# Optimization experiments

Measured on AMD Instinct MI355X. Metric: run time of the kernel, lower is better.

The kernel has to match this reference:

```python
import jax, jax.numpy as jnp
import numpy as np

VOCAB = 8192  # upper bound on integer values appearing in features


def setup_inputs() -> dict:
    key = jax.random.key(0)
    # [B, L] integer codes; each row is treated as a SET of values (duplicates ignored)
    features = jax.random.randint(key, (4096, 256), 0, VOCAB, dtype=jnp.int32)
    return {"features": features}


def reference(features) -> jnp.ndarray:
    # np.intersect1d / np.union1d compute set intersection/union of unique values.
    # Equivalent vectorized form: binary presence matrix P[i, v] = 1 iff value v in row i.
    B, L = features.shape
    rows = jnp.arange(B)[:, None]                                  # [B, 1]
    presence = jnp.zeros((B, VOCAB), jnp.float32).at[rows, features].set(1.0)  # [B, V]
    inter = presence @ presence.T                                  # [B, B] |A_i & A_j|
    sizes = presence.sum(axis=1)                                   # [B]    |A_i|
    union = sizes[:, None] + sizes[None, :] - inter                # [B, B] |A_i | A_j|
    # original returns -intersection/union (note the negation), 0 when union == 0
    sim = jnp.where(union != 0, -inter / jnp.where(union != 0, union, 1.0), 0.0)
    return sim
```

## Files before the change

### kernel.cpp

```cpp
#include <hip/hip_runtime.h>
#include <stdint.h>

#define B_ROWS 4096
#define L_FEAT 256
#define VOCAB  8192
#define FRAG   1024
#define KCHUNKS (VOCAB / 64)
#define GBYTES  (KCHUNKS * FRAG)
#define NSTEP  128

typedef __attribute__((ext_vector_type(4)))  int   intx4;
typedef __attribute__((ext_vector_type(8)))  int   intx8;
typedef __attribute__((ext_vector_type(4)))  float floatx4;
typedef __attribute__((ext_vector_type(16))) float floatx16;

__device__ __forceinline__ intx8 widen(intx4 v) {
  return __builtin_shufflevector(v, v, 0, 1, 2, 3, -1, -1, -1, -1);
}

__global__ __launch_bounds__(256) void presence_kernel(
    const int* __restrict__ f,
    uint32_t* __restrict__ P,
    float* __restrict__ sizes) {
  __shared__ uint32_t rw[4][VOCAB / 8];
  const int rbase = blockIdx.x * 4;
  const int tid = threadIdx.x;

  uint4* rp4 = (uint4*)&rw[0][0];
  const uint4 z = make_uint4(0u, 0u, 0u, 0u);
  #pragma unroll
  for (int j = 0; j < 4; ++j) rp4[tid + j * 256] = z;
  __syncthreads();

  #pragma unroll
  for (int r = 0; r < 4; ++r) {
    const int v = f[(rbase + r) * L_FEAT + tid];
    atomicOr(&rw[r][v >> 3], 0x2u << ((v & 7) * 4));
  }
  __syncthreads();

  const int g = blockIdx.x >> 3;
  const int slotBase = (blockIdx.x & 7) * 4;
  char* Pg = (char*)P + (size_t)g * GBYTES;
  #pragma unroll
  for (int j = 0; j < 4; ++j) {
    const int c  = tid + j * 256;
    const int kc = c >> 3, h = (c >> 2) & 1, ro = c & 3;
    const uint4 val = *(const uint4*)&rw[ro][kc * 8 + h * 4];
    *(uint4*)(Pg + kc * FRAG + (slotBase + ro + 32 * h) * 16) = val;
  }

  const int w = tid >> 6, lane = tid & 63;
  const uint4* sp4 = (const uint4*)&rw[w][0];
  int cnt = 0;
  #pragma unroll
  for (int q = 0; q < 4; ++q) {
    const uint4 x = sp4[lane + q * 64];
    cnt += __popc(x.x & 0x22222222u) + __popc(x.y & 0x22222222u) +
           __popc(x.z & 0x22222222u) + __popc(x.w & 0x22222222u);
  }
  #pragma unroll
  for (int off = 32; off > 0; off >>= 1) cnt += __shfl_down(cnt, off);
  if (lane == 0) sizes[rbase + w] = (float)cnt;
}

__global__ __launch_bounds__(256, 2) void gemm_kernel(
    const unsigned char* __restrict__ P,
    const float* __restrict__ sizes,
    float* __restrict__ out) {
  int bid = blockIdx.x;
  bid = (bid & 7) * 66 + (bid >> 3);
  int b = bid, sy = 0, rem = 122;
  while (b >= rem) { b -= rem; ++sy; rem -= 16; }
  int by, bx;
  if (b < 10) {
    int ly = 0, r2 = 4;
    while (b >= r2) { b -= r2; ++ly; --r2; }
    by = sy * 4 + ly; bx = sy * 4 + ly + b;
  } else {
    const int t = b - 10;
    const int sx = sy + 1 + (t >> 4);
    const int l = t & 15;
    by = sy * 4 + (l >> 2); bx = sx * 4 + (l & 3);
  }

  const int tid  = threadIdx.x;
  const int wave = tid >> 6, lane = tid & 63;
  const int wm = wave >> 1, wn = wave & 1;
  const int r31 = lane & 31, khalf = lane >> 5;

  const int iB = by * 128 + wm * 64;
  const int jB = bx * 128 + wn * 64;

  const unsigned char* pA0 = P + (size_t)(by * 4 + wm * 2 + 0) * GBYTES + lane * 16;
  const unsigned char* pA1 = P + (size_t)(by * 4 + wm * 2 + 1) * GBYTES + lane * 16;
  const unsigned char* pB0 = P + (size_t)(bx * 4 + wn * 2 + 0) * GBYTES + lane * 16;
  const unsigned char* pB1 = P + (size_t)(bx * 4 + wn * 2 + 1) * GBYTES + lane * 16;

  floatx16 acc[2][2];
  #pragma unroll
  for (int ai = 0; ai < 2; ++ai)
    #pragma unroll
    for (int ci = 0; ci < 2; ++ci)
      #pragma unroll
      for (int e = 0; e < 16; ++e) acc[ai][ci][e] = 0.f;

  intx4 a0[8], a1[8], b0[8], b1[8];

  #pragma unroll
  for (int j = 0; j < 8; ++j) {
    a0[j] = *(const intx4*)(pA0 + j * FRAG);
    a1[j] = *(const intx4*)(pA1 + j * FRAG);
    b0[j] = *(const intx4*)(pB0 + j * FRAG);
    b1[j] = *(const intx4*)(pB1 + j * FRAG);
  }
  pA0 += 8 * FRAG; pA1 += 8 * FRAG; pB0 += 8 * FRAG; pB1 += 8 * FRAG;

  #define STEP(j)                                                             \
    {                                                                         \
      const intx8 A0 = widen(a0[j]), A1 = widen(a1[j]);                       \
      const intx8 B0 = widen(b0[j]), B1 = widen(b1[j]);                       \
      acc[0][0] = __builtin_amdgcn_mfma_scale_f32_32x32x64_f8f6f4(            \
          A0, B0, acc[0][0], 4, 4, 0, 127, 0, 127);                           \
      acc[0][1] = __builtin_amdgcn_mfma_scale_f32_32x32x64_f8f6f4(            \
          A0, B1, acc[0][1], 4, 4, 0, 127, 0, 127);                           \
      acc[1][0] = __builtin_amdgcn_mfma_scale_f32_32x32x64_f8f6f4(            \
          A1, B0, acc[1][0], 4, 4, 0, 127, 0, 127);                           \
      acc[1][1] = __builtin_amdgcn_mfma_scale_f32_32x32x64_f8f6f4(            \
          A1, B1, acc[1][1], 4, 4, 0, 127, 0, 127);                           \
    }
  #define PREF(j)                                                             \
    {                                                                         \
      a0[j] = *(const intx4*)(pA0 + (j) * FRAG);                              \
      a1[j] = *(const intx4*)(pA1 + (j) * FRAG);                              \
      b0[j] = *(const intx4*)(pB0 + (j) * FRAG);                              \
      b1[j] = *(const intx4*)(pB1 + (j) * FRAG);                              \
    }

  for (int i = 0; i < 15; ++i) {
    STEP(0) PREF(0)
    STEP(1) PREF(1)
    STEP(2) PREF(2)
    STEP(3) PREF(3)
    STEP(4) PREF(4)
    STEP(5) PREF(5)
    STEP(6) PREF(6)
    STEP(7) PREF(7)
    pA0 += 8 * FRAG; pA1 += 8 * FRAG; pB0 += 8 * FRAG; pB1 += 8 * FRAG;
  }
  STEP(0) STEP(1) STEP(2) STEP(3)
  STEP(4) STEP(5) STEP(6) STEP(7)

  #pragma unroll
  for (int tm = 0; tm < 2; ++tm) {
    const int rowb = iB + tm * 32 + 4 * khalf;
    #pragma unroll
    for (int tn = 0; tn < 2; ++tn) {
      const int colb = jB + tn * 32 + r31;
      const float sj = sizes[colb];
      #pragma unroll
      for (int q = 0; q < 4; ++q) {
        const int rq = rowb + 8 * q;
        floatx4 tv;
        #pragma unroll
        for (int j = 0; j < 4; ++j) {
          const float inter = acc[tm][tn][4 * q + j];
          const float u = sizes[rq + j] + sj - inter;
          tv[j] = (u != 0.f) ? (-inter / u) : 0.f;
        }
        __builtin_nontemporal_store(tv[0], &out[(size_t)(rq + 0) * B_ROWS + colb]);
        __builtin_nontemporal_store(tv[1], &out[(size_t)(rq + 1) * B_ROWS + colb]);
        __builtin_nontemporal_store(tv[2], &out[(size_t)(rq + 2) * B_ROWS + colb]);
        __builtin_nontemporal_store(tv[3], &out[(size_t)(rq + 3) * B_ROWS + colb]);
        __builtin_nontemporal_store(tv, (floatx4*)&out[(size_t)colb * B_ROWS + rq]);
      }
    }
  }
}

extern "C" void kernel_launch(void* const* d_in, const int* in_sizes, int n_in,
                              void* d_out, int out_size, void* d_ws, size_t ws_size,
                              hipStream_t stream) {
  const int* features = (const int*)d_in[0];
  float* out = (float*)d_out;
  uint32_t* P = (uint32_t*)d_ws;
  float* sizes = (float*)((char*)d_ws + (size_t)(B_ROWS / 32) * GBYTES);

  presence_kernel<<<B_ROWS / 4, 256, 0, stream>>>(features, P, sizes);
  gemm_kernel<<<528, 256, 0, stream>>>((const unsigned char*)P, sizes, out);
}
```

Baseline: 166.1 us.

## Stage GEMM operands through LDS with async global_load_lds triple buffering

Replaces the register-prefetch pipeline, which held eight K-steps of operands in VGPRs, with per-wave triple-buffered LDS staging filled by asynchronous global_load_lds copies and gated by vmcnt waits. MFMA issue is wrapped in s_setprio, and launch bounds are raised to three blocks per SU. The aim is to free registers for higher occupancy and hide memory latency through more resident waves. The cost is that prefetch depth drops from eight steps to two, and the loop adds extra LDS round-trips. The last two iterations fetch wrapped-around addresses that are never used.

New measurement: 169.6 us. +2.1%, slower.

```diff
diff --git a/kernel.cpp b/kernel.cpp
--- a/kernel.cpp
+++ b/kernel.cpp
@@ -16,6 +16,12 @@
 
 __device__ __forceinline__ intx8 widen(intx4 v) {
   return __builtin_shufflevector(v, v, 0, 1, 2, 3, -1, -1, -1, -1);
+}
+
+__device__ __forceinline__ void async_copy16(const void* gsrc, void* ldst) {
+  __builtin_amdgcn_global_load_lds(
+      (const __attribute__((address_space(1))) void*)gsrc,
+      (__attribute__((address_space(3))) void*)ldst, 16, 0, 0);
 }
 
 __global__ __launch_bounds__(256) void presence_kernel(
@@ -64,7 +70,7 @@
   if (lane == 0) sizes[rbase + w] = (float)cnt;
 }
 
-__global__ __launch_bounds__(256, 2) void gemm_kernel(
+__global__ __launch_bounds__(256, 3) void gemm_kernel(
     const unsigned char* __restrict__ P,
     const float* __restrict__ sizes,
     float* __restrict__ out) {
@@ -84,6 +90,8 @@
     by = sy * 4 + (l >> 2); bx = sx * 4 + (l & 3);
   }
 
+  __shared__ __align__(16) unsigned char lds[4][3][4096];
+
   const int tid  = threadIdx.x;
   const int wave = tid >> 6, lane = tid & 63;
   const int wm = wave >> 1, wn = wave & 1;
@@ -97,6 +105,8 @@
   const unsigned char* pB0 = P + (size_t)(bx * 4 + wn * 2 + 0) * GBYTES + lane * 16;
   const unsigned char* pB1 = P + (size_t)(bx * 4 + wn * 2 + 1) * GBYTES + lane * 16;
 
+  unsigned char* myLds = &lds[wave][0][0];
+
   floatx16 acc[2][2];
   #pragma unroll
   for (int ai = 0; ai < 2; ++ai)
@@ -105,51 +115,45 @@
       #pragma unroll
       for (int e = 0; e < 16; ++e) acc[ai][ci][e] = 0.f;
 
-  intx4 a0[8], a1[8], b0[8], b1[8];
-
-  #pragma unroll
-  for (int j = 0; j < 8; ++j) {
-    a0[j] = *(const intx4*)(pA0 + j * FRAG);
-    a1[j] = *(const intx4*)(pA1 + j * FRAG);
-    b0[j] = *(const intx4*)(pB0 + j * FRAG);
-    b1[j] = *(const intx4*)(pB1 + j * FRAG);
-  }
-  pA0 += 8 * FRAG; pA1 += 8 * FRAG; pB0 += 8 * FRAG; pB1 += 8 * FRAG;
-
-  #define STEP(j)                                                             \
+  #define STAGE(slot, koff)                                                   \
     {                                                                         \
-      const intx8 A0 = widen(a0[j]), A1 = widen(a1[j]);                       \
-      const intx8 B0 = widen(b0[j]), B1 = widen(b1[j]);                       \
-      acc[0][0] = __builtin_amdgcn_mfma_scale_f32_32x32x64_f8f6f4(            \
-          A0, B0, acc[0][0], 4, 4, 0, 127, 0, 127);                           \
-      acc[0][1] = __builtin_amdgcn_mfma_scale_f32_32x32x64_f8f6f4(            \
-          A0, B1, acc[0][1], 4, 4, 0, 127, 0, 127);                           \
-      acc[1][0] = __builtin_amdgcn_mfma_scale_f32_32x32x64_f8f6f4(            \
-          A1, B0, acc[1][0], 4, 4, 0, 127, 0, 127);                           \
-      acc[1][1] = __builtin_amdgcn_mfma_scale_f32_32x32x64_f8f6f4(            \
-          A1, B1, acc[1][1], 4, 4, 0, 127, 0, 127);                           \
-    }
-  #define PREF(j)                                                             \
-    {                                                                         \
-      a0[j] = *(const intx4*)(pA0 + (j) * FRAG);                              \
-      a1[j] = *(const intx4*)(pA1 + (j) * FRAG);                              \
-      b0[j] = *(const intx4*)(pB0 + (j) * FRAG);                              \
-      b1[j] = *(const intx4*)(pB1 + (j) * FRAG);                              \
+      async_copy16(pA0 + (koff), myLds + (slot) * 4096 + 0);                  \
+      async_copy16(pA1 + (koff), myLds + (slot) * 4096 + 1024);               \
+      async_copy16(pB0 + (koff), myLds + (slot) * 4096 + 2048);               \
+      async_copy16(pB1 + (koff), myLds + (slot) * 4096 + 3072);               \
     }
 
-  for (int i = 0; i < 15; ++i) {
-    STEP(0) PREF(0)
-    STEP(1) PREF(1)
-    STEP(2) PREF(2)
-    STEP(3) PREF(3)
-    STEP(4) PREF(4)
-    STEP(5) PREF(5)
-    STEP(6) PREF(6)
-    STEP(7) PREF(7)
-    pA0 += 8 * FRAG; pA1 += 8 * FRAG; pB0 += 8 * FRAG; pB1 += 8 * FRAG;
+  STAGE(0, 0);
+  STAGE(1, FRAG);
+
+  int cur = 0, pre = 2;
+  for (int i = 0; i < NSTEP; ++i) {
+    STAGE(pre, (size_t)(((i + 2) & (NSTEP - 1))) * FRAG);
+
+    asm volatile("s_waitcnt vmcnt(8)" ::: "memory");
+
+    const unsigned char* s = myLds + cur * 4096 + lane * 16;
+    const intx4 A4_0 = *(const intx4*)(s);
+    const intx4 A4_1 = *(const intx4*)(s + 1024);
+    const intx4 B4_0 = *(const intx4*)(s + 2048);
+    const intx4 B4_1 = *(const intx4*)(s + 3072);
+    const intx8 A0 = widen(A4_0), A1 = widen(A4_1);
+    const intx8 B0 = widen(B4_0), B1 = widen(B4_1);
+
+    __builtin_amdgcn_s_setprio(1);
+    acc[0][0] = __builtin_amdgcn_mfma_scale_f32_32x32x64_f8f6f4(
+        A0, B0, acc[0][0], 4, 4, 0, 127, 0, 127);
+    acc[0][1] = __builtin_amdgcn_mfma_scale_f32_32x32x64_f8f6f4(
+        A0, B1, acc[0][1], 4, 4, 0, 127, 0, 127);
+    acc[1][0] = __builtin_amdgcn_mfma_scale_f32_32x32x64_f8f6f4(
+        A1, B0, acc[1][0], 4, 4, 0, 127, 0, 127);
+    acc[1][1] = __builtin_amdgcn_mfma_scale_f32_32x32x64_f8f6f4(
+        A1, B1, acc[1][1], 4, 4, 0, 127, 0, 127);
+    __builtin_amdgcn_s_setprio(0);
+
+    cur = (cur == 2) ? 0 : cur + 1;
+    pre = (pre == 2) ? 0 : pre + 1;
   }
-  STEP(0) STEP(1) STEP(2) STEP(3)
-  STEP(4) STEP(5) STEP(6) STEP(7)
 
   #pragma unroll
   for (int tm = 0; tm < 2; ++tm) {
```
